# Kernel tuning notes

Measured on AMD Instinct MI355X. Metric: run time of the kernel, lower is better.

Reference implementation:

```python
import jax, jax.numpy as jnp
import numpy as np
import math

# dims matching init_kwargs
B, N, CS, CZ = 1, 512, 384, 128
H, C, PQ, PV = 8, 128, 8, 8
INF, EPS = 1e5, 1e-8

# ---- quaternion / motor helpers (PGA motor encoded as [qw,qx,qy,qz,tx,ty,tz,0]) ----

def quat_conj(q):
    return q * jnp.array([1.0, -1.0, -1.0, -1.0], q.dtype)

def quat_mul(a, b):
    aw, ax, ay, az = jnp.split(a, 4, -1)
    bw, bx, by, bz = jnp.split(b, 4, -1)
    return jnp.concatenate([
        aw*bw - ax*bx - ay*by - az*bz,
        aw*bx + ax*bw + ay*bz - az*by,
        aw*by - ax*bz + ay*bw + az*bx,
        aw*bz + ax*by - ay*bx + az*bw], -1)

def quat_rotate(q, v):
    qv = q[..., 1:]
    uv = jnp.cross(qv, v)
    uuv = jnp.cross(qv, uv)
    return v + 2.0 * (q[..., :1] * uv + uuv)

def point_trafo(p, q, t):
    # p [...,K,3]; rigid transform by frame motor, homogeneous 4-vector out
    pp = quat_rotate(q, p) + t
    return jnp.concatenate([pp, jnp.ones_like(pp[..., :1])], -1)

def mv_transform(mv, q, t):
    # versor sandwich on a 16-dim multivector: three rotatable 3-vector blocks,
    # the point block (7:10, weight at 10) also translates; slots 0 and 10:16 invariant
    s0 = mv[..., 0:1]
    v1 = quat_rotate(q, mv[..., 1:4])
    v2 = quat_rotate(q, mv[..., 4:7])
    w = mv[..., 10:11]
    p = quat_rotate(q, mv[..., 7:10]) + w * t
    return jnp.concatenate([s0, v1, v2, p, mv[..., 10:16]], -1)

def mv_transform_inv(mv, q, t):
    qc = quat_conj(q)
    s0 = mv[..., 0:1]
    v1 = quat_rotate(qc, mv[..., 1:4])
    v2 = quat_rotate(qc, mv[..., 4:7])
    w = mv[..., 10:11]
    p = quat_rotate(qc, mv[..., 7:10] - w * t)
    return jnp.concatenate([s0, v1, v2, p, mv[..., 10:16]], -1)


def _forward(s, g, z, T, mask, W_q, b_q, W_kv, b_kv, W_qp, b_qp, W_kp, b_kp,
             W_vg, b_vg, W_mg, W_b, b_b, W_dz, b_dz, head_weights,
             softmax_weights, W_out, b_out, W_geo):
    T8 = T[..., :8]                                      # extract_motor
    qn = T8[..., :4]
    qn = qn / jnp.sqrt(jnp.sum(qn**2, -1, keepdims=True) + EPS)
    tr = T8[..., 4:7]

    q = (s @ W_q + b_q).reshape(B, N, H, C)
    kv = (s @ W_kv + b_kv).reshape(B, N, H, 2 * C)
    k, v = kv[..., :C], kv[..., C:]

    def make_pts(W, bb):
        # split into 3 chunks + stack(dim=-1) == reshape(...,3,HP).swapaxes
        p = (s @ W + bb).reshape(B, N, 3, H * PQ).swapaxes(-1, -2)  # [B,N,HP,3]
        p4 = point_trafo(p, qn[:, :, None, :], tr[:, :, None, :])
        return p4.reshape(B, N, H, PQ, 4)

    q_pts = make_pts(W_qp, b_qp)
    k_pts = make_pts(W_kp, b_kp)

    v_g = (s @ W_vg + b_vg).reshape(B, N, PV, 16)
    v_g = jnp.einsum('oi,bnic->bnoc', W_mg,
                     jnp.concatenate([v_g, g], -2)).reshape(B, N, H, PV, 16)

    bias = jnp.einsum('bijz,zh->bhij', z, W_b) + b_b[None, :, None, None]
    a = jnp.einsum('bihc,bjhc->bhij', q, k) * math.sqrt(1.0 / (3 * C))
    a = a + math.sqrt(1.0 / 3.0) * bias

    disp = q_pts[:, :, None, :, :, :3] - k_pts[:, None, :, :, :, :3]  # [B,N,N,H,P,3]
    pt = jnp.sum(disp**2, -1)                                         # [B,N,N,H,P]
    hw = jax.nn.softplus(head_weights) * math.sqrt(1.0 / (3 * (PQ * 9.0 / 2)))
    pt = -0.5 * jnp.sum(pt * hw[None, None, None, :, None], -1)       # [B,N,N,H]

    sq_mask = INF * (mask[:, :, None] * mask[:, None, :] - 1.0)
    a = a + pt.transpose(0, 3, 1, 2) + sq_mask[:, None]
    a = jax.nn.softmax(softmax_weights[None, :, None, None] * a, axis=-1)

    o = jnp.einsum('bhij,bjhc->bihc', a, v)                           # [B,N,H,C]

    qb, tb = qn[:, :, None, None, :], tr[:, :, None, None, :]
    vg_glob = mv_transform(v_g, qb, tb)
    o_g = jnp.einsum('bhij,bjhpc->bihpc', a, vg_glob)
    o_g = mv_transform_inv(o_g, qb, tb)                               # [B,N,H,PV,16]
    n1 = jnp.sqrt(jnp.sum(o_g[..., :10]**2, -1) + EPS)
    n2 = jnp.sqrt(jnp.sum(o_g[..., 10:]**2, -1) + EPS)
    o_g_norm = jnp.stack([n1, n2], -1)                                # [B,N,H,PV,2]

    # local relative frame features (8 per head)
    q_rel = quat_mul(quat_conj(qn)[:, :, None, :], qn[:, None, :, :])
    t_rel = quat_rotate(quat_conj(qn)[:, :, None, :], tr[:, None, :, :] - tr[:, :, None, :])
    rel = jnp.concatenate([q_rel, t_rel, jnp.zeros_like(t_rel[..., :1])], -1)  # [B,N,N,8]
    o_rel = jnp.einsum('bhij,bijc->bihc', a, rel)

    o_pair = jnp.einsum('bhij,bijc->bihc', a, z @ W_dz + b_dz)        # [B,N,H,CZ//4]

    feats = jnp.concatenate([o_pair, o, o_rel,
                             o_g.reshape(B, N, H, PV * 16),
                             o_g_norm.reshape(B, N, H, PV * 2)], -1).reshape(B, N, -1)
    s_out = feats @ W_out + b_out                                     # [B,N,CS]
    g_out = jnp.einsum('oi,bnic->bnoc', W_geo, o_g.reshape(B, N, H * PV, 16))
    return s_out, g_out


def setup_inputs() -> dict:
    key = jax.random.key(0)
    ks = jax.random.split(key, 32)
    def rn(i, shape, sc=1.0):
        return sc * jax.random.normal(ks[i], shape, jnp.float32)
    s = rn(0, (B, N, CS))
    g = rn(1, (B, N, PV, 16))
    z = rn(2, (B, N, N, CZ))
    Traw = rn(3, (B, N, 16))
    qn = Traw[..., :4]
    qn = qn / jnp.sqrt(jnp.sum(qn**2, -1, keepdims=True) + 1e-8)
    T = Traw.at[..., :4].set(qn).at[..., 4:7].multiply(3.0).at[..., 7:].set(0.0)
    mask = jnp.ones((B, N), jnp.float32)
    w = 0.02
    CAT = H * (CZ // 4 + C + 8 + PV * 18)   # 2496
    return dict(
        s=s, g=g, z=z, T=T, mask=mask,
        W_q=rn(4, (CS, H * C), w), b_q=jnp.zeros((H * C,), jnp.float32),
        W_kv=rn(5, (CS, 2 * H * C), w), b_kv=jnp.zeros((2 * H * C,), jnp.float32),
        W_qp=rn(6, (CS, H * PQ * 3), w), b_qp=jnp.zeros((H * PQ * 3,), jnp.float32),
        W_kp=rn(7, (CS, H * PQ * 3), w), b_kp=jnp.zeros((H * PQ * 3,), jnp.float32),
        W_vg=rn(8, (CS, PV * 16), w), b_vg=jnp.zeros((PV * 16,), jnp.float32),
        W_mg=rn(9, (H * PV, 2 * PV), 0.1),
        W_b=rn(10, (CZ, H), w), b_b=jnp.zeros((H,), jnp.float32),
        W_dz=rn(11, (CZ, CZ // 4), w), b_dz=jnp.zeros((CZ // 4,), jnp.float32),
        head_weights=-2.0 + 0.3 * rn(12, (H,)),
        softmax_weights=jnp.ones((H,), jnp.float32) + 0.1 * rn(13, (H,)),
        W_out=rn(14, (CAT, CS), w), b_out=jnp.zeros((CS,), jnp.float32),
        W_geo=rn(15, (PV, H * PV), 0.1))


def reference(s, g, z, T, mask, W_q, b_q, W_kv, b_kv, W_qp, b_qp, W_kp, b_kp,
              W_vg, b_vg, W_mg, W_b, b_b, W_dz, b_dz, head_weights,
              softmax_weights, W_out, b_out, W_geo):
    return _forward(s, g, z, T, mask, W_q, b_q, W_kv, b_kv, W_qp, b_qp, W_kp,
                    b_kp, W_vg, b_vg, W_mg, W_b, b_b, W_dz, b_dz, head_weights,
                    softmax_weights, W_out, b_out, W_geo)
```

## Files before the change

### kernel.cpp

```cpp
#include <hip/hip_runtime.h>
#include <math.h>

#define NN 512
#define CSD 384
#define CZD 128
#define HD 8
#define CD 128
#define EPSV 1e-8f
#define INFV 100000.0f

#define OFF_QN    ((size_t)0)
#define OFF_TR    ((size_t)2048)
#define OFF_ROWT  ((size_t)4096)
#define OFF_COLT  ((size_t)8192)
#define OFF_SB    ((size_t)12288)
#define OFF_QBUF  ((size_t)45056)
#define OFF_KV    ((size_t)569344)
#define OFF_QPR   ((size_t)1617920)
#define OFF_KPR   ((size_t)1716224)
#define OFF_VGR   ((size_t)1814528)
#define OFF_ZB    ((size_t)1880064)
#define OFF_A     ((size_t)3977216)
#define OFF_AMH   ((size_t)6074368)
#define OFF_AML   ((size_t)7122944)
#define OFF_UH    ((size_t)8171520)
#define OFF_UL    ((size_t)8499200)
#define OFF_VH    ((size_t)8826880)
#define OFF_VL    ((size_t)9154560)
#define OFF_VPH   ((size_t)9482240)
#define OFF_VPL   ((size_t)10006528)
#define OFF_OB0   ((size_t)10530816)
#define OFF_OB1   ((size_t)11055104)
#define OFF_OG0   ((size_t)11579392)
#define OFF_OG1   ((size_t)12103680)
#define OFF_FH    ((size_t)12627968)
#define OFF_FL    ((size_t)13266944)
#define OFF_PS    ((size_t)13905920)
#define OFF_SH    ((size_t)15085568)
#define OFF_SL    ((size_t)15183872)
#define OFF_WTH   ((size_t)15282176)
#define OFF_WTL   ((size_t)15970304)
#define OFF_WOH   ((size_t)16658432)
#define OFF_WOL   ((size_t)17137664)

typedef __attribute__((ext_vector_type(4))) float f32x4;
typedef __attribute__((ext_vector_type(8))) short bf16x8;
typedef __attribute__((ext_vector_type(4))) short s16x4;
typedef unsigned short u16;

__device__ __forceinline__ void qrot(const float q[4], const float* v, float* out) {
    float qw = q[0], qx = q[1], qy = q[2], qz = q[3];
    float ux = qy*v[2] - qz*v[1];
    float uy = qz*v[0] - qx*v[2];
    float uz = qx*v[1] - qy*v[0];
    float uux = qy*uz - qz*uy;
    float uuy = qz*ux - qx*uz;
    float uuz = qx*uy - qy*ux;
    out[0] = v[0] + 2.0f*(qw*ux + uux);
    out[1] = v[1] + 2.0f*(qw*uy + uuy);
    out[2] = v[2] + 2.0f*(qw*uz + uuz);
}

__device__ __forceinline__ void cvt2(float x, u16& h, u16& lo) {
    unsigned u = __float_as_uint(x);
    unsigned r = (u + 0x7FFFu + ((u >> 16) & 1u)) >> 16;
    h = (u16)r;
    float hf = __uint_as_float(r << 16);
    float lf = x - hf;
    unsigned u2 = __float_as_uint(lf);
    unsigned r2 = (u2 + 0x7FFFu + ((u2 >> 16) & 1u)) >> 16;
    lo = (u16)r2;
}
__device__ __forceinline__ float bf2f(u16 h) { return __uint_as_float((unsigned)h << 16); }

#define MFMA3(acc, avh, avl, bvh, bvl) \
    acc = __builtin_amdgcn_mfma_f32_16x16x32_bf16(avh, bvh, acc, 0, 0, 0); \
    acc = __builtin_amdgcn_mfma_f32_16x16x32_bf16(avh, bvl, acc, 0, 0, 0); \
    acc = __builtin_amdgcn_mfma_f32_16x16x32_bf16(avl, bvh, acc, 0, 0, 0);


__global__ __launch_bounds__(256) void k_split(
    const float* __restrict__ s, const float* __restrict__ W_q, const float* __restrict__ W_kv,
    const float* __restrict__ W_qp, const float* __restrict__ W_kp, const float* __restrict__ W_vg,
    const float* __restrict__ W_out,
    u16* __restrict__ sh_, u16* __restrict__ sl_,
    u16* __restrict__ WTh, u16* __restrict__ WTl,
    u16* __restrict__ WOh, u16* __restrict__ WOl)
{
    __shared__ float tile[64*68];
    int task = blockIdx.z, bx = blockIdx.x, by = blockIdx.y, t = threadIdx.x;
    if (task == 0) {
        if (by >= 6) return;
        const float* W; int ldn, sn0;
        if (bx < 16)      { W = W_q;  ldn = 1024; sn0 = bx*64; }
        else if (bx < 48) { W = W_kv; ldn = 2048; sn0 = (bx-16)*64; }
        else if (bx < 51) { W = W_qp; ldn = 192;  sn0 = (bx-48)*64; }
        else if (bx < 54) { W = W_kp; ldn = 192;  sn0 = (bx-51)*64; }
        else              { W = W_vg; ldn = 128;  sn0 = (bx-54)*64; }
        int k0 = by*64;
        #pragma unroll
        for (int lp = 0; lp < 4; lp++) {
            int kk = (t>>4) + lp*16, nn = (t&15)*4;
            float4 v = *(const float4*)(W + (size_t)(k0+kk)*ldn + sn0 + nn);
            tile[kk*68+nn]=v.x; tile[kk*68+nn+1]=v.y; tile[kk*68+nn+2]=v.z; tile[kk*68+nn+3]=v.w;
        }
        __syncthreads();
        #pragma unroll
        for (int lp = 0; lp < 4; lp++) {
            int nn = (t>>4) + lp*16, kk4 = (t&15)*4;
            s16x4 vh, vl;
            #pragma unroll
            for (int e = 0; e < 4; e++) {
                u16 h, lo; cvt2(tile[(kk4+e)*68 + nn], h, lo);
                vh[e] = (short)h; vl[e] = (short)lo;
            }
            size_t o = (size_t)(bx*64 + nn)*384 + k0 + kk4;
            *(s16x4*)(WTh + o) = vh;
            *(s16x4*)(WTl + o) = vl;
        }
    } else if (task == 1) {
        if (bx >= 6 || by >= 39) return;
        int n0 = bx*64, k0 = by*64;
        #pragma unroll
        for (int lp = 0; lp < 4; lp++) {
            int kk = (t>>4) + lp*16, nn = (t&15)*4;
            float4 v = *(const float4*)(W_out + (size_t)(k0+kk)*384 + n0 + nn);
            tile[kk*68+nn]=v.x; tile[kk*68+nn+1]=v.y; tile[kk*68+nn+2]=v.z; tile[kk*68+nn+3]=v.w;
        }
        __syncthreads();
        #pragma unroll
        for (int lp = 0; lp < 4; lp++) {
            int nn = (t>>4) + lp*16, kk4 = (t&15)*4;
            s16x4 vh, vl;
            #pragma unroll
            for (int e = 0; e < 4; e++) {
                u16 h, lo; cvt2(tile[(kk4+e)*68 + nn], h, lo);
                vh[e] = (short)h; vl[e] = (short)lo;
            }
            size_t o = (size_t)(n0 + nn)*2496 + k0 + kk4;
            *(s16x4*)(WOh + o) = vh;
            *(s16x4*)(WOl + o) = vl;
        }
    } else {
        if (bx >= 8 || by >= 6) return;
        int m0 = bx*64, k0 = by*64;
        #pragma unroll
        for (int lp = 0; lp < 4; lp++) {
            int row = (t>>4) + lp*16, c4 = (t&15)*4;
            float4 v = *(const float4*)(s + (size_t)(m0+row)*384 + k0 + c4);
            s16x4 vh, vl;
            u16 h, lo;
            cvt2(v.x,h,lo); vh[0]=(short)h; vl[0]=(short)lo;
            cvt2(v.y,h,lo); vh[1]=(short)h; vl[1]=(short)lo;
            cvt2(v.z,h,lo); vh[2]=(short)h; vl[2]=(short)lo;
            cvt2(v.w,h,lo); vh[3]=(short)h; vl[3]=(short)lo;
            size_t o = (size_t)(m0+row)*384 + k0 + c4;
            *(s16x4*)(sh_ + o) = vh;
            *(s16x4*)(sl_ + o) = vl;
        }
    }
}

__global__ __launch_bounds__(256) void k_proj_all(
    const u16* __restrict__ sh_, const u16* __restrict__ sl_,
    const u16* __restrict__ WTh, const u16* __restrict__ WTl,
    const float* __restrict__ b_q,  float* __restrict__ qbuf,
    const float* __restrict__ b_kv, float* __restrict__ kvb,
    const float* __restrict__ b_qp, float* __restrict__ qpr,
    const float* __restrict__ b_kp, float* __restrict__ kpr,
    const float* __restrict__ b_vg, float* __restrict__ vgr)
{
    int ny = blockIdx.y;
    const float* bias; float* C; int N, n0, base;
    if (ny < 16)      { bias=b_q;  C=qbuf; N=1024; n0=ny*64;      base=0; }
    else if (ny < 48) { bias=b_kv; C=kvb;  N=2048; n0=(ny-16)*64; base=1024; }
    else if (ny < 51) { bias=b_qp; C=qpr;  N=192;  n0=(ny-48)*64; base=3072; }
    else if (ny < 54) { bias=b_kp; C=kpr;  N=192;  n0=(ny-51)*64; base=3264; }
    else              { bias=b_vg; C=vgr;  N=128;  n0=(ny-54)*64; base=3456; }
    int m0 = blockIdx.x*64;
    int t = threadIdx.x, w = t>>6, l = t&63, g = l>>4, li = l&15;
    const u16* Ah = sh_ + (size_t)(m0 + w*16 + li)*384 + g*8;
    const u16* Al = sl_ + (size_t)(m0 + w*16 + li)*384 + g*8;
    const u16* Bh0 = WTh + (size_t)(base + n0 + li)*384 + g*8;
    const u16* Bl0 = WTl + (size_t)(base + n0 + li)*384 + g*8;
    f32x4 acc[4] = {};
    for (int ks = 0; ks < 12; ks++) {
        bf16x8 avh = *(const bf16x8*)(Ah + ks*32);
        bf16x8 avl = *(const bf16x8*)(Al + ks*32);
        #pragma unroll
        for (int c = 0; c < 4; c++) {
            bf16x8 bvh = *(const bf16x8*)(Bh0 + (size_t)c*16*384 + ks*32);
            bf16x8 bvl = *(const bf16x8*)(Bl0 + (size_t)c*16*384 + ks*32);
            MFMA3(acc[c], avh, avl, bvh, bvl);
        }
    }
    #pragma unroll
    for (int c = 0; c < 4; c++) {
        int col = n0 + c*16 + li;
        float bb = bias[col];
        #pragma unroll
        for (int r = 0; r < 4; r++) {
            int row = m0 + w*16 + g*4 + r;
            C[(size_t)row*N + col] = acc[c][r] + bb;
        }
    }
}

__global__ __launch_bounds__(256) void k_geo(
    const float* __restrict__ T,
    const float* __restrict__ qpr, const float* __restrict__ kpr,
    const float* __restrict__ vgr, const float* __restrict__ g,
    const float* __restrict__ W_mg,
    const float* __restrict__ qbuf, const float* __restrict__ kvb,
    const float* __restrict__ hwraw, const float* __restrict__ b_b,
    float* __restrict__ qn, float* __restrict__ tr,
    u16* __restrict__ Uh, u16* __restrict__ Ul,
    u16* __restrict__ Vh, u16* __restrict__ Vl,
    float* __restrict__ rowt, float* __restrict__ colt,
    u16* __restrict__ Vph, u16* __restrict__ Vpl)
{
    __shared__ float s_q[4];
    __shared__ float s_t[3];
    __shared__ float s_qpts[192], s_kpts[192];
    __shared__ float s_Qsq[8], s_Ksq[8];
    int n = blockIdx.x, t = threadIdx.x;
    if (t == 0) {
        float q0=T[n*16+0], q1=T[n*16+1], q2=T[n*16+2], q3=T[n*16+3];
        float inv = 1.0f/sqrtf(q0*q0+q1*q1+q2*q2+q3*q3 + EPSV);
        float a0=q0*inv, a1=q1*inv, a2=q2*inv, a3=q3*inv;
        s_q[0]=a0; s_q[1]=a1; s_q[2]=a2; s_q[3]=a3;
        float u0=T[n*16+4], u1=T[n*16+5], u2=T[n*16+6];
        s_t[0]=u0; s_t[1]=u1; s_t[2]=u2;
        qn[n*4+0]=a0; qn[n*4+1]=a1; qn[n*4+2]=a2; qn[n*4+3]=a3;
        tr[n*3+0]=u0; tr[n*3+1]=u1; tr[n*3+2]=u2;
    }
    __syncthreads();
    float q[4]={s_q[0],s_q[1],s_q[2],s_q[3]};
    float t0=s_t[0], t1=s_t[1], t2=s_t[2];
    if (t < 128) {
        int m = t & 63;
        const float* raw = (t < 64) ? qpr : kpr;
        float p[3] = {raw[n*192 + m], raw[n*192 + 64 + m], raw[n*192 + 128 + m]};
        float r[3]; qrot(q,p,r);
        r[0]+=t0; r[1]+=t1; r[2]+=t2;
        float* dp = (t<64) ? s_qpts : s_kpts;
        dp[m*3+0]=r[0]; dp[m*3+1]=r[1]; dp[m*3+2]=r[2];
        float ss = r[0]*r[0]+r[1]*r[1]+r[2]*r[2];
        ss += __shfl_down(ss,4,8);
        ss += __shfl_down(ss,2,8);
        ss += __shfl_down(ss,1,8);
        if ((m&7)==0) ((t<64)?s_Qsq:s_Ksq)[m>>3] = ss;
    } else if (t < 192) {
        int o = t - 128;
        float in[16];
        #pragma unroll
        for (int c=0;c<16;c++){
            float acc=0.0f;
            #pragma unroll
            for (int i=0;i<8;i++)  acc += W_mg[o*16+i]*vgr[n*128+i*16+c];
            #pragma unroll
            for (int i=8;i<16;i++) acc += W_mg[o*16+i]*g[n*128+(i-8)*16+c];
            in[c]=acc;
        }
        float out[16];
        out[0]=in[0];
        qrot(q,in+1,out+1);
        qrot(q,in+4,out+4);
        float w=in[10];
        qrot(q,in+7,out+7);
        out[7]+=w*t0; out[8]+=w*t1; out[9]+=w*t2;
        #pragma unroll
        for (int c=10;c<16;c++) out[c]=in[c];
        int h=o>>3, pp=o&7;
        size_t vb = ((size_t)(h*512+n))*256 + 128 + pp*16;
        #pragma unroll
        for (int c=0;c<16;c++) {
            u16 hh, ll; cvt2(out[c], hh, ll);
            Vph[vb+c]=hh; Vpl[vb+c]=ll;
        }
    }
    #pragma unroll
    for (int l=0;l<4;l++){
        int f = t + l*256; int h = f>>7, c = f&127;
        u16 hh, ll; cvt2(kvb[(size_t)n*2048 + h*256 + 128 + c], hh, ll);
        Vph[((size_t)(h*512+n))*256 + c] = hh;
        Vpl[((size_t)(h*512+n))*256 + c] = ll;
    }
    __syncthreads();
    #pragma unroll
    for (int h = 0; h < 8; h++) {
        float hwv = log1pf(expf(hwraw[h])) * 0.09622504486493763f;
        if (t < 160) {
            float u, v;
            if (t < 128) {
                u = 0.05103103630798287f * qbuf[(size_t)n*1024 + h*128 + t];
                v = kvb[(size_t)n*2048 + h*256 + t];
            } else if (t < 152) {
                int d = t - 128;
                u = hwv * s_qpts[h*24 + d];
                v = s_kpts[h*24 + d];
            } else { u = 0.0f; v = 0.0f; }
            size_t o = ((size_t)h*512 + n)*160 + t;
            u16 hh, ll;
            cvt2(u, hh, ll); Uh[o]=hh; Ul[o]=ll;
            cvt2(v, hh, ll); Vh[o]=hh; Vl[o]=ll;
        }
        if (t == 160) rowt[h*512+n] = -0.5f*hwv*s_Qsq[h] + 0.5773502691896258f*b_b[h] - INFV;
        if (t == 161) colt[h*512+n] = -0.5f*hwv*s_Ksq[h];
    }
}

__global__ __launch_bounds__(128) void k_zb(const float* __restrict__ z,
        const float* __restrict__ W_b, float* __restrict__ zb) {
    __shared__ float zt[64*132];
    __shared__ float part[8*64];
    int i = blockIdx.x, j0 = blockIdx.y*64;
    int t = threadIdx.x;
    #pragma unroll
    for (int l = 0; l < 16; l++) {
        int f = t + l*128;
        int row = f >> 5, c4 = (f & 31) << 2;
        float4 v = *(const float4*)(z + ((size_t)(i*NN) + j0 + row)*CZD + c4);
        *(float4*)(zt + row*132 + c4) = v;
    }
    __syncthreads();
    int w = t >> 6, j = t & 63;
    int cbase = w*64;
    float acc[8] = {};
    #pragma unroll
    for (int c16 = 0; c16 < 16; c16++) {
        float4 v = *(const float4*)(zt + j*132 + cbase + c16*4);
        int c = cbase + c16*4;
        #pragma unroll
        for (int h = 0; h < 8; h++)
            acc[h] += v.x*W_b[(c+0)*8+h] + v.y*W_b[(c+1)*8+h]
                    + v.z*W_b[(c+2)*8+h] + v.w*W_b[(c+3)*8+h];
    }
    if (w == 1) {
        #pragma unroll
        for (int h = 0; h < 8; h++) part[h*64 + j] = acc[h];
    }
    __syncthreads();
    if (w == 0) {
        #pragma unroll
        for (int h = 0; h < 8; h++)
            zb[((size_t)h*512 + i)*512 + j0 + j] = acc[h] + part[h*64 + j];
    }
}

__global__ __launch_bounds__(256) void k_scorefill(
        const u16* __restrict__ Uh, const u16* __restrict__ Ul,
        const u16* __restrict__ Vh, const u16* __restrict__ Vl,
        const float* __restrict__ rowt, const float* __restrict__ colt,
        const float* __restrict__ zb, const float* __restrict__ mask,
        const float* __restrict__ sw, float* __restrict__ Am) {
    int h = blockIdx.z;
    int m0 = blockIdx.x*64, n0 = blockIdx.y*64;
    int t = threadIdx.x, w = t>>6, l = t&63, g = l>>4, li = l&15;
    const u16* Ah = Uh + ((size_t)h*512 + m0 + w*16 + li)*160 + g*8;
    const u16* Al = Ul + ((size_t)h*512 + m0 + w*16 + li)*160 + g*8;
    const u16* Bh0 = Vh + ((size_t)h*512 + n0 + li)*160 + g*8;
    const u16* Bl0 = Vl + ((size_t)h*512 + n0 + li)*160 + g*8;
    f32x4 acc[4] = {};
    #pragma unroll
    for (int ks = 0; ks < 5; ks++) {
        bf16x8 avh = *(const bf16x8*)(Ah + ks*32);
        bf16x8 avl = *(const bf16x8*)(Al + ks*32);
        #pragma unroll
        for (int c = 0; c < 4; c++) {
            bf16x8 bvh = *(const bf16x8*)(Bh0 + (size_t)c*16*160 + ks*32);
            bf16x8 bvl = *(const bf16x8*)(Bl0 + (size_t)c*16*160 + ks*32);
            MFMA3(acc[c], avh, avl, bvh, bvl);
        }
    }
    float swh = sw[h];
    #pragma unroll
    for (int c = 0; c < 4; c++) {
        int j = n0 + c*16 + li;
        float ct = colt[h*512 + j];
        float mj = mask[j];
        #pragma unroll
        for (int r = 0; r < 4; r++) {
            int i = m0 + w*16 + g*4 + r;
            float rt = rowt[h*512 + i];
            float mi = mask[i]*INFV;
            float zv = zb[((size_t)h*512 + i)*512 + j];
            Am[((size_t)h*512 + i)*512 + j] =
                (acc[c][r] + rt + ct + 0.5773502691896258f*zv + mi*mj)*swh;
        }
    }
}

__global__ __launch_bounds__(256) void k_softmax(const float* __restrict__ Am,
        u16* __restrict__ Amh, u16* __restrict__ Aml,
        const float* __restrict__ qn, const float* __restrict__ tr, float* __restrict__ S) {
    __shared__ float red[8];
    __shared__ float sred[4][8];
    int row = blockIdx.x;
    const float* p = Am + (size_t)row*512;
    int t = threadIdx.x;
    float x0 = p[t], x1 = p[t+256];
    float m = fmaxf(x0, x1);
    #pragma unroll
    for (int o = 32; o > 0; o >>= 1) m = fmaxf(m, __shfl_xor(m, o));
    int wv = t >> 6, ln = t & 63;
    if (ln == 0) red[wv] = m;
    __syncthreads();
    m = fmaxf(fmaxf(red[0], red[1]), fmaxf(red[2], red[3]));
    float e0 = expf(x0 - m), e1 = expf(x1 - m);
    float sm = e0 + e1;
    #pragma unroll
    for (int o = 32; o > 0; o >>= 1) sm += __shfl_xor(sm, o);
    __syncthreads();
    if (ln == 0) red[4 + wv] = sm;
    __syncthreads();
    float inv = 1.0f / (red[4]+red[5]+red[6]+red[7]);
    float a0 = e0*inv, a1 = e1*inv;
    u16 hh, ll;
    cvt2(a0, hh, ll); Amh[(size_t)row*512 + t] = hh;     Aml[(size_t)row*512 + t] = ll;
    cvt2(a1, hh, ll); Amh[(size_t)row*512 + t+256] = hh; Aml[(size_t)row*512 + t+256] = ll;
    float4 q0 = *(const float4*)(qn + t*4);
    float4 q1 = *(const float4*)(qn + (t+256)*4);
    float acc[8];
    acc[0] = a0*q0.x + a1*q1.x;
    acc[1] = a0*q0.y + a1*q1.y;
    acc[2] = a0*q0.z + a1*q1.z;
    acc[3] = a0*q0.w + a1*q1.w;
    acc[4] = a0*tr[t*3+0] + a1*tr[(t+256)*3+0];
    acc[5] = a0*tr[t*3+1] + a1*tr[(t+256)*3+1];
    acc[6] = a0*tr[t*3+2] + a1*tr[(t+256)*3+2];
    acc[7] = a0 + a1;
    #pragma unroll
    for (int c = 0; c < 8; c++) {
        #pragma unroll
        for (int o = 32; o > 0; o >>= 1) acc[c] += __shfl_xor(acc[c], o);
    }
    if (ln == 0) {
        #pragma unroll
        for (int c = 0; c < 8; c++) sred[wv][c] = acc[c];
    }
    __syncthreads();
    if (t < 8) {
        int h = row >> 9, i = row & 511;
        S[i*64 + h*8 + t] = sred[0][t]+sred[1][t]+sred[2][t]+sred[3][t];
    }
}

__global__ __launch_bounds__(256) void k_apply(
        const u16* __restrict__ Amh, const u16* __restrict__ Aml,
        const u16* __restrict__ Vph, const u16* __restrict__ Vpl,
        float* __restrict__ ob0, float* __restrict__ ob1,
        float* __restrict__ og0, float* __restrict__ og1) {
    __shared__ u16 sBh[2][64*48];
    __shared__ u16 sBl[2][64*48];
    int m0 = blockIdx.x*64;
    int n0 = blockIdx.y*64;
    int h = blockIdx.z & 7, js = blockIdx.z >> 3;
    int t = threadIdx.x, w = t>>6, l = t&63, g = l>>4, li = l&15;
    int jl = t>>3, c8 = (t&7)*8;
    int jsw = jl ^ (((c8>>3)&3)<<3);
    const u16* Ah = Amh + ((size_t)h*512 + m0 + w*16 + li)*512 + js*256 + g*8;
    const u16* Al = Aml + ((size_t)h*512 + m0 + w*16 + li)*512 + js*256 + g*8;
    f32x4 acc[4] = {};
    {
        const u16* srcH = Vph + ((size_t)h*512 + js*256 + jl)*256 + n0 + c8;
        const u16* srcL = Vpl + ((size_t)h*512 + js*256 + jl)*256 + n0 + c8;
        bf16x8 vh = *(const bf16x8*)srcH;
        bf16x8 vl = *(const bf16x8*)srcL;
        #pragma unroll
        for (int e = 0; e < 8; e++) {
            sBh[0][(c8+e)*48 + jsw] = (u16)vh[e];
            sBl[0][(c8+e)*48 + jsw] = (u16)vl[e];
        }
    }
    __syncthreads();
    for (int kc = 0; kc < 8; kc++) {
        int cur = kc & 1;
        if (kc + 1 < 8) {
            int koff = js*256 + (kc+1)*32;
            const u16* srcH = Vph + ((size_t)h*512 + koff + jl)*256 + n0 + c8;
            const u16* srcL = Vpl + ((size_t)h*512 + koff + jl)*256 + n0 + c8;
            bf16x8 vh = *(const bf16x8*)srcH;
            bf16x8 vl = *(const bf16x8*)srcL;
            #pragma unroll
            for (int e = 0; e < 8; e++) {
                sBh[cur^1][(c8+e)*48 + jsw] = (u16)vh[e];
                sBl[cur^1][(c8+e)*48 + jsw] = (u16)vl[e];
            }
        }
        bf16x8 avh = *(const bf16x8*)(Ah + kc*32);
        bf16x8 avl = *(const bf16x8*)(Al + kc*32);
        #pragma unroll
        for (int c = 0; c < 4; c++) {
            int col = c*16 + li;
            int gp = g ^ ((col>>3)&3);
            bf16x8 bvh = *(const bf16x8*)(&sBh[cur][col*48 + gp*8]);
            bf16x8 bvl = *(const bf16x8*)(&sBl[cur][col*48 + gp*8]);
            MFMA3(acc[c], avh, avl, bvh, bvl);
        }
        __syncthreads();
    }
    float* obuf = js ? ob1 : ob0;
    float* og   = js ? og1 : og0;
    #pragma unroll
    for (int c = 0; c < 4; c++) {
        int col = n0 + c*16 + li;
        float* base = (col < 128) ? (obuf + h*128 + col) : (og + h*128 + col - 128);
        #pragma unroll
        for (int r = 0; r < 4; r++) {
            int i = m0 + w*16 + g*4 + r;
            base[(size_t)i*1024] = acc[c][r];
        }
    }
}

__global__ __launch_bounds__(256) void k_azfin(
    const u16* __restrict__ Amh, const u16* __restrict__ Aml, const float* __restrict__ z,
    const float* __restrict__ ob0, const float* __restrict__ ob1,
    const float* __restrict__ og0, const float* __restrict__ og1,
    const float* __restrict__ W_dz, const float* __restrict__ b_dz,
    const float* __restrict__ S, const float* __restrict__ qn, const float* __restrict__ tr,
    const float* __restrict__ W_geo,
    u16* __restrict__ fh, u16* __restrict__ fl, float* __restrict__ outg)
{
    __shared__ float aT[512*8];
    __shared__ float part[3*1024];
    __shared__ float s_az[1024];
    __shared__ float s_og[1024];
    int i = blockIdx.x, t = threadIdx.x;
    #pragma unroll
    for (int l = 0; l < 16; l++) {
        int f = t + l*256;
        int h = f >> 9, j = f & 511;
        size_t idx = ((size_t)h*512 + i)*512 + j;
        aT[j*8 + h] = bf2f(Amh[idx]) + bf2f(Aml[idx]);
    }
    __syncthreads();
    int c2 = t & 63, quarter = t >> 6;
    int jb = quarter*128;
    float acc[8][2] = {};
    for (int j = jb; j < jb+128; j++) {
        float2 zv = *(const float2*)(z + ((size_t)(i*NN) + j)*CZD + c2*2);
        float4 a0 = *(const float4*)(aT + j*8);
        float4 a1 = *(const float4*)(aT + j*8 + 4);
        acc[0][0] += a0.x*zv.x; acc[0][1] += a0.x*zv.y;
        acc[1][0] += a0.y*zv.x; acc[1][1] += a0.y*zv.y;
        acc[2][0] += a0.z*zv.x; acc[2][1] += a0.z*zv.y;
        acc[3][0] += a0.w*zv.x; acc[3][1] += a0.w*zv.y;
        acc[4][0] += a1.x*zv.x; acc[4][1] += a1.x*zv.y;
        acc[5][0] += a1.y*zv.x; acc[5][1] += a1.y*zv.y;
        acc[6][0] += a1.z*zv.x; acc[6][1] += a1.z*zv.y;
        acc[7][0] += a1.w*zv.x; acc[7][1] += a1.w*zv.y;
    }
    if (quarter > 0) {
        #pragma unroll
        for (int h = 0; h < 8; h++) {
            part[(quarter-1)*1024 + h*128 + c2*2 + 0] = acc[h][0];
            part[(quarter-1)*1024 + h*128 + c2*2 + 1] = acc[h][1];
        }
    }
    __syncthreads();
    if (quarter == 0) {
        #pragma unroll
        for (int h = 0; h < 8; h++) {
            #pragma unroll
            for (int d = 0; d < 2; d++) {
                s_az[h*128 + c2*2 + d] = acc[h][d] + part[h*128 + c2*2 + d]
                          + part[1024 + h*128 + c2*2 + d] + part[2048 + h*128 + c2*2 + d];
            }
        }
    }
    __syncthreads();
    size_t fb = (size_t)i*2496;
    u16 hh, ll;
    #pragma unroll
    for (int l = 0; l < 4; l++) {
        int ff = t + l*256; int h = ff>>7, c = ff&127;
        float v = ob0[(size_t)i*1024 + h*128 + c] + ob1[(size_t)i*1024 + h*128 + c];
        cvt2(v, hh, ll); fh[fb + h*312 + 32 + c] = hh; fl[fb + h*312 + 32 + c] = ll;
    }
    {
        int h = t >> 5, cdz = t & 31;
        float a2 = b_dz[cdz];
        #pragma unroll 4
        for (int zc = 0; zc < 128; zc++) a2 += s_az[h*128 + zc]*W_dz[zc*32 + cdz];
        cvt2(a2, hh, ll); fh[fb + h*312 + cdz] = hh; fl[fb + h*312 + cdz] = ll;
    }
    float qc0=qn[i*4], qc1=-qn[i*4+1], qc2=-qn[i*4+2], qc3=-qn[i*4+3];
    float t0=tr[i*3], t1=tr[i*3+1], t2=tr[i*3+2];
    if (t < 64) {
        int h = t >> 3, p = t & 7;
        const float* a0 = og0 + (size_t)i*1024 + h*128 + p*16;
        const float* a1 = og1 + (size_t)i*1024 + h*128 + p*16;
        float in[16];
        #pragma unroll
        for (int c=0;c<16;c++) in[c]=a0[c]+a1[c];
        float qc[4]={qc0,qc1,qc2,qc3};
        float out[16];
        out[0]=in[0];
        qrot(qc,in+1,out+1);
        qrot(qc,in+4,out+4);
        float w=in[10];
        float tmp[3]={in[7]-w*t0, in[8]-w*t1, in[9]-w*t2};
        qrot(qc,tmp,out+7);
        #pragma unroll
        for (int c2x=10;c2x<16;c2x++) out[c2x]=in[c2x];
        float n1=EPSV, n2=EPSV;
        #pragma unroll
        for (int c2x=0;c2x<10;c2x++) n1 += out[c2x]*out[c2x];
        #pragma unroll
        for (int c2x=10;c2x<16;c2x++) n2 += out[c2x]*out[c2x];
        n1=sqrtf(n1); n2=sqrtf(n2);
        #pragma unroll
        for (int c2x=0;c2x<16;c2x++){
            cvt2(out[c2x], hh, ll);
            fh[fb + h*312+168+p*16+c2x] = hh; fl[fb + h*312+168+p*16+c2x] = ll;
            s_og[t*16+c2x]=out[c2x];
        }
        cvt2(n1, hh, ll); fh[fb + h*312+296+p*2]   = hh; fl[fb + h*312+296+p*2]   = ll;
        cvt2(n2, hh, ll); fh[fb + h*312+296+p*2+1] = hh; fl[fb + h*312+296+p*2+1] = ll;
    } else if (t < 72) {
        int h = t - 64;
        const float* Sr = S + i*64 + h*8;
        float b0=Sr[0], b1=Sr[1], b2=Sr[2], b3=Sr[3];
        float o0 = qc0*b0 - qc1*b1 - qc2*b2 - qc3*b3;
        float o1 = qc0*b1 + qc1*b0 + qc2*b3 - qc3*b2;
        float o2 = qc0*b2 - qc1*b3 + qc2*b0 + qc3*b1;
        float o3 = qc0*b3 + qc1*b2 - qc2*b1 + qc3*b0;
        float A = Sr[7];
        float v[3]={Sr[4]-A*t0, Sr[5]-A*t1, Sr[6]-A*t2};
        float qc[4]={qc0,qc1,qc2,qc3};
        float r[3]; qrot(qc,v,r);
        cvt2(o0,hh,ll);  fh[fb+h*312+160]=hh; fl[fb+h*312+160]=ll;
        cvt2(o1,hh,ll);  fh[fb+h*312+161]=hh; fl[fb+h*312+161]=ll;
        cvt2(o2,hh,ll);  fh[fb+h*312+162]=hh; fl[fb+h*312+162]=ll;
        cvt2(o3,hh,ll);  fh[fb+h*312+163]=hh; fl[fb+h*312+163]=ll;
        cvt2(r[0],hh,ll);fh[fb+h*312+164]=hh; fl[fb+h*312+164]=ll;
        cvt2(r[1],hh,ll);fh[fb+h*312+165]=hh; fl[fb+h*312+165]=ll;
        cvt2(r[2],hh,ll);fh[fb+h*312+166]=hh; fl[fb+h*312+166]=ll;
        fh[fb+h*312+167]=0; fl[fb+h*312+167]=0;
    }
    __syncthreads();
    if (t < 128) {
        int o = (t>>4) & 7, c = t & 15;
        float a3 = 0.0f;
        #pragma unroll 4
        for (int i2=0;i2<64;i2++) a3 += W_geo[o*64+i2]*s_og[i2*16+c];
        outg[(size_t)i*128 + o*16 + c] = a3;
    }
}

__global__ __launch_bounds__(256) void k_sout(
        const u16* __restrict__ fh, const u16* __restrict__ fl,
        const u16* __restrict__ WOh, const u16* __restrict__ WOl,
        float* __restrict__ Ps) {
    int m0 = blockIdx.x*64, n0 = blockIdx.y*64, kz = blockIdx.z;
    int t = threadIdx.x, w = t>>6, l = t&63, g = l>>4, li = l&15;
    const u16* Ah = fh + (size_t)(m0 + w*16 + li)*2496 + kz*416 + g*8;
    const u16* Al = fl + (size_t)(m0 + w*16 + li)*2496 + kz*416 + g*8;
    const u16* Bh0 = WOh + (size_t)(n0 + li)*2496 + kz*416 + g*8;
    const u16* Bl0 = WOl + (size_t)(n0 + li)*2496 + kz*416 + g*8;
    f32x4 acc[4] = {};
    for (int ks = 0; ks < 13; ks++) {
        bf16x8 avh = *(const bf16x8*)(Ah + ks*32);
        bf16x8 avl = *(const bf16x8*)(Al + ks*32);
        #pragma unroll
        for (int c = 0; c < 4; c++) {
            bf16x8 bvh = *(const bf16x8*)(Bh0 + (size_t)c*16*2496 + ks*32);
            bf16x8 bvl = *(const bf16x8*)(Bl0 + (size_t)c*16*2496 + ks*32);
            MFMA3(acc[c], avh, avl, bvh, bvl);
        }
    }
    float* slab = Ps + (size_t)kz*512*384;
    #pragma unroll
    for (int c = 0; c < 4; c++) {
        int col = n0 + c*16 + li;
        #pragma unroll
        for (int r = 0; r < 4; r++) {
            int row = m0 + w*16 + g*4 + r;
            slab[(size_t)row*CSD + col] = acc[c][r];
        }
    }
}

__global__ __launch_bounds__(256) void k_sout_red(const float* __restrict__ Ps,
        const float* __restrict__ b_out, float* __restrict__ out) {
    int idx = (blockIdx.x*256 + threadIdx.x)*4;
    float4 s = *(const float4*)(b_out + (idx % 384));
    #pragma unroll
    for (int kz = 0; kz < 6; kz++) {
        float4 p = *(const float4*)(Ps + (size_t)kz*196608 + idx);
        s.x += p.x; s.y += p.y; s.z += p.z; s.w += p.w;
    }
    *(float4*)(out + idx) = s;
}


extern "C" void kernel_launch(void* const* d_in, const int* in_sizes, int n_in,
                              void* d_out, int out_size, void* d_ws, size_t ws_size,
                              hipStream_t stream) {
    const float* s     = (const float*)d_in[0];
    const float* g     = (const float*)d_in[1];
    const float* z     = (const float*)d_in[2];
    const float* T     = (const float*)d_in[3];
    const float* mask  = (const float*)d_in[4];
    const float* W_q   = (const float*)d_in[5];
    const float* b_q   = (const float*)d_in[6];
    const float* W_kv  = (const float*)d_in[7];
    const float* b_kv  = (const float*)d_in[8];
    const float* W_qp  = (const float*)d_in[9];
    const float* b_qp  = (const float*)d_in[10];
    const float* W_kp  = (const float*)d_in[11];
    const float* b_kp  = (const float*)d_in[12];
    const float* W_vg  = (const float*)d_in[13];
    const float* b_vg  = (const float*)d_in[14];
    const float* W_mg  = (const float*)d_in[15];
    const float* W_b   = (const float*)d_in[16];
    const float* b_b   = (const float*)d_in[17];
    const float* W_dz  = (const float*)d_in[18];
    const float* b_dz  = (const float*)d_in[19];
    const float* hw    = (const float*)d_in[20];
    const float* sw    = (const float*)d_in[21];
    const float* W_out = (const float*)d_in[22];
    const float* b_out = (const float*)d_in[23];
    const float* W_geo = (const float*)d_in[24];

    float* ws   = (float*)d_ws;
    float* out  = (float*)d_out;

    float* qn   = ws + OFF_QN;
    float* tr   = ws + OFF_TR;
    float* rowt = ws + OFF_ROWT;
    float* colt = ws + OFF_COLT;
    float* Sbuf = ws + OFF_SB;
    float* qbuf = ws + OFF_QBUF;
    float* kvb  = ws + OFF_KV;
    float* qpr  = ws + OFF_QPR;
    float* kpr  = ws + OFF_KPR;
    float* vgr  = ws + OFF_VGR;
    float* zb   = ws + OFF_ZB;
    float* Am   = ws + OFF_A;
    u16* Amh    = (u16*)(ws + OFF_AMH);
    u16* Aml    = (u16*)(ws + OFF_AML);
    u16* Uh     = (u16*)(ws + OFF_UH);
    u16* Ul     = (u16*)(ws + OFF_UL);
    u16* Vh     = (u16*)(ws + OFF_VH);
    u16* Vl     = (u16*)(ws + OFF_VL);
    u16* Vph    = (u16*)(ws + OFF_VPH);
    u16* Vpl    = (u16*)(ws + OFF_VPL);
    float* ob0  = ws + OFF_OB0;
    float* ob1  = ws + OFF_OB1;
    float* og0  = ws + OFF_OG0;
    float* og1  = ws + OFF_OG1;
    u16* fh     = (u16*)(ws + OFF_FH);
    u16* fl     = (u16*)(ws + OFF_FL);
    float* Ps   = ws + OFF_PS;
    u16* sh_    = (u16*)(ws + OFF_SH);
    u16* sl_    = (u16*)(ws + OFF_SL);
    u16* WTh    = (u16*)(ws + OFF_WTH);
    u16* WTl    = (u16*)(ws + OFF_WTL);
    u16* WOh    = (u16*)(ws + OFF_WOH);
    u16* WOl    = (u16*)(ws + OFF_WOL);

    k_split<<<dim3(56,39,3),256,0,stream>>>(s,W_q,W_kv,W_qp,W_kp,W_vg,W_out,
                                            sh_,sl_,WTh,WTl,WOh,WOl);
    k_proj_all<<<dim3(8,56),256,0,stream>>>(sh_,sl_,WTh,WTl,
                                            b_q,qbuf, b_kv,kvb, b_qp,qpr, b_kp,kpr, b_vg,vgr);
    k_geo<<<NN,256,0,stream>>>(T,qpr,kpr,vgr,g,W_mg,qbuf,kvb,hw,b_b,
                               qn,tr,Uh,Ul,Vh,Vl,rowt,colt,Vph,Vpl);
    k_zb<<<dim3(NN,8),128,0,stream>>>(z,W_b,zb);
    k_scorefill<<<dim3(8,8,8),256,0,stream>>>(Uh,Ul,Vh,Vl,rowt,colt,zb,mask,sw,Am);
    k_softmax<<<4096,256,0,stream>>>(Am,Amh,Aml,qn,tr,Sbuf);
    k_apply<<<dim3(8,4,16),256,0,stream>>>(Amh,Aml,Vph,Vpl,ob0,ob1,og0,og1);
    k_azfin<<<NN,256,0,stream>>>(Amh,Aml,z,ob0,ob1,og0,og1,W_dz,b_dz,Sbuf,qn,tr,W_geo,
                                 fh,fl, out + (size_t)NN*CSD);
    k_sout<<<dim3(8,6,6),256,0,stream>>>(fh,fl,WOh,WOl,Ps);
    k_sout_red<<<192,256,0,stream>>>(Ps,b_out,out);
}
```

Measured before the change: 409.6 us.

## Split attention-weighted z reduction into parallel kernel and rework k_zb with register weights

The A·z reduction that k_azfin did in one block per row is moved into a new k_az kernel. It splits the j dimension into four chunks across a 512x4 grid and writes partial sums to a workspace buffer, which k_azfin then adds up. This raises parallelism on the largest z read, at the cost of an extra launch and a partial-sum round trip through memory. Separately, k_zb drops the shared-memory staging and keeps the W_b slice in registers, reducing with wavefront shuffles over 256-thread blocks.

```diff
diff --git a/kernel.cpp b/kernel.cpp
--- a/kernel.cpp
+++ b/kernel.cpp
@@ -42,6 +42,7 @@
 #define OFF_WTL   ((size_t)15970304)
 #define OFF_WOH   ((size_t)16658432)
 #define OFF_WOL   ((size_t)17137664)
+#define OFF_AZP   ((size_t)17616896)
 
 typedef __attribute__((ext_vector_type(4))) float f32x4;
 typedef __attribute__((ext_vector_type(8))) short bf16x8;
@@ -310,41 +311,33 @@
     }
 }
 
-__global__ __launch_bounds__(128) void k_zb(const float* __restrict__ z,
+__global__ __launch_bounds__(256) void k_zb(const float* __restrict__ z,
         const float* __restrict__ W_b, float* __restrict__ zb) {
-    __shared__ float zt[64*132];
-    __shared__ float part[8*64];
-    int i = blockIdx.x, j0 = blockIdx.y*64;
-    int t = threadIdx.x;
-    #pragma unroll
-    for (int l = 0; l < 16; l++) {
-        int f = t + l*128;
-        int row = f >> 5, c4 = (f & 31) << 2;
-        float4 v = *(const float4*)(z + ((size_t)(i*NN) + j0 + row)*CZD + c4);
-        *(float4*)(zt + row*132 + c4) = v;
-    }
-    __syncthreads();
-    int w = t >> 6, j = t & 63;
-    int cbase = w*64;
-    float acc[8] = {};
-    #pragma unroll
-    for (int c16 = 0; c16 < 16; c16++) {
-        float4 v = *(const float4*)(zt + j*132 + cbase + c16*4);
-        int c = cbase + c16*4;
-        #pragma unroll
-        for (int h = 0; h < 8; h++)
-            acc[h] += v.x*W_b[(c+0)*8+h] + v.y*W_b[(c+1)*8+h]
-                    + v.z*W_b[(c+2)*8+h] + v.w*W_b[(c+3)*8+h];
-    }
-    if (w == 1) {
-        #pragma unroll
-        for (int h = 0; h < 8; h++) part[h*64 + j] = acc[h];
-    }
-    __syncthreads();
-    if (w == 0) {
-        #pragma unroll
-        for (int h = 0; h < 8; h++)
-            zb[((size_t)h*512 + i)*512 + j0 + j] = acc[h] + part[h*64 + j];
+    int i = blockIdx.x, j0 = blockIdx.y*128;
+    int t = threadIdx.x, w = t>>6, l = t&63;
+    int jj = l>>5, c4 = (l&31)<<2;
+    float wb[4][8];
+    #pragma unroll
+    for (int e=0;e<4;e++)
+        #pragma unroll
+        for (int h=0;h<8;h++) wb[e][h] = W_b[(c4+e)*8 + h];
+    int jbase = j0 + w*32 + jj;
+    const float* zp = z + ((size_t)i*512 + jbase)*128 + c4;
+    for (int k = 0; k < 16; k++) {
+        float4 v = *(const float4*)(zp + (size_t)k*256);
+        float acc[8];
+        #pragma unroll
+        for (int h=0;h<8;h++)
+            acc[h] = v.x*wb[0][h] + v.y*wb[1][h] + v.z*wb[2][h] + v.w*wb[3][h];
+        #pragma unroll
+        for (int h=0;h<8;h++) {
+            #pragma unroll
+            for (int m=16;m>0;m>>=1) acc[h] += __shfl_xor(acc[h], m);
+        }
+        if ((l&31) < 8) {
+            int h = l&31;
+            zb[((size_t)h*512 + i)*512 + jbase + k*2] = acc[h];
+        }
     }
 }
 
@@ -443,6 +436,59 @@
     if (t < 8) {
         int h = row >> 9, i = row & 511;
         S[i*64 + h*8 + t] = sred[0][t]+sred[1][t]+sred[2][t]+sred[3][t];
+    }
+}
+
+__global__ __launch_bounds__(256) void k_az(
+        const u16* __restrict__ Amh, const u16* __restrict__ Aml,
+        const float* __restrict__ z, float* __restrict__ azp) {
+    __shared__ float aT[128*12];
+    __shared__ float part[3*1024];
+    int i = blockIdx.x, jq = blockIdx.y, j0 = jq*128;
+    int t = threadIdx.x;
+    #pragma unroll
+    for (int l2 = 0; l2 < 4; l2++) {
+        int f = t + l2*256;
+        int h = f >> 7, jl = f & 127;
+        size_t idx = ((size_t)h*512 + i)*512 + j0 + jl;
+        aT[jl*12 + h] = bf2f(Amh[idx]) + bf2f(Aml[idx]);
+    }
+    __syncthreads();
+    int c2 = t & 63, sub = t >> 6;
+    int jb = sub*32;
+    float acc[8][2] = {};
+    for (int jo = 0; jo < 32; jo++) {
+        int j = jb + jo;
+        float2 zv = *(const float2*)(z + ((size_t)i*512 + j0 + j)*128 + c2*2);
+        float4 a0 = *(const float4*)(aT + j*12);
+        float4 a1 = *(const float4*)(aT + j*12 + 4);
+        acc[0][0] += a0.x*zv.x; acc[0][1] += a0.x*zv.y;
+        acc[1][0] += a0.y*zv.x; acc[1][1] += a0.y*zv.y;
+        acc[2][0] += a0.z*zv.x; acc[2][1] += a0.z*zv.y;
+        acc[3][0] += a0.w*zv.x; acc[3][1] += a0.w*zv.y;
+        acc[4][0] += a1.x*zv.x; acc[4][1] += a1.x*zv.y;
+        acc[5][0] += a1.y*zv.x; acc[5][1] += a1.y*zv.y;
+        acc[6][0] += a1.z*zv.x; acc[6][1] += a1.z*zv.y;
+        acc[7][0] += a1.w*zv.x; acc[7][1] += a1.w*zv.y;
+    }
+    if (sub > 0) {
+        #pragma unroll
+        for (int h = 0; h < 8; h++) {
+            part[(sub-1)*1024 + h*128 + c2*2 + 0] = acc[h][0];
+            part[(sub-1)*1024 + h*128 + c2*2 + 1] = acc[h][1];
+        }
+    }
+    __syncthreads();
+    if (sub == 0) {
+        float* dst = azp + ((size_t)jq*512 + i)*1024;
+        #pragma unroll
+        for (int h = 0; h < 8; h++) {
+            #pragma unroll
+            for (int d = 0; d < 2; d++) {
+                dst[h*128 + c2*2 + d] = acc[h][d] + part[h*128 + c2*2 + d]
+                          + part[1024 + h*128 + c2*2 + d] + part[2048 + h*128 + c2*2 + d];
+            }
+        }
     }
 }
 
@@ -515,7 +561,7 @@
 }
 
 __global__ __launch_bounds__(256) void k_azfin(
-    const u16* __restrict__ Amh, const u16* __restrict__ Aml, const float* __restrict__ z,
+    const float* __restrict__ azp,
     const float* __restrict__ ob0, const float* __restrict__ ob1,
     const float* __restrict__ og0, const float* __restrict__ og1,
     const float* __restrict__ W_dz, const float* __restrict__ b_dz,
@@ -523,52 +569,14 @@
     const float* __restrict__ W_geo,
     u16* __restrict__ fh, u16* __restrict__ fl, float* __restrict__ outg)
 {
-    __shared__ float aT[512*8];
-    __shared__ float part[3*1024];
     __shared__ float s_az[1024];
     __shared__ float s_og[1024];
     int i = blockIdx.x, t = threadIdx.x;
     #pragma unroll
-    for (int l = 0; l < 16; l++) {
-        int f = t + l*256;
-        int h = f >> 9, j = f & 511;
-        size_t idx = ((size_t)h*512 + i)*512 + j;
-        aT[j*8 + h] = bf2f(Amh[idx]) + bf2f(Aml[idx]);
-    }
-    __syncthreads();
-    int c2 = t & 63, quarter = t >> 6;
-    int jb = quarter*128;
-    float acc[8][2] = {};
-    for (int j = jb; j < jb+128; j++) {
-        float2 zv = *(const float2*)(z + ((size_t)(i*NN) + j)*CZD + c2*2);
-        float4 a0 = *(const float4*)(aT + j*8);
-        float4 a1 = *(const float4*)(aT + j*8 + 4);
-        acc[0][0] += a0.x*zv.x; acc[0][1] += a0.x*zv.y;
-        acc[1][0] += a0.y*zv.x; acc[1][1] += a0.y*zv.y;
-        acc[2][0] += a0.z*zv.x; acc[2][1] += a0.z*zv.y;
-        acc[3][0] += a0.w*zv.x; acc[3][1] += a0.w*zv.y;
-        acc[4][0] += a1.x*zv.x; acc[4][1] += a1.x*zv.y;
-        acc[5][0] += a1.y*zv.x; acc[5][1] += a1.y*zv.y;
-        acc[6][0] += a1.z*zv.x; acc[6][1] += a1.z*zv.y;
-        acc[7][0] += a1.w*zv.x; acc[7][1] += a1.w*zv.y;
-    }
-    if (quarter > 0) {
-        #pragma unroll
-        for (int h = 0; h < 8; h++) {
-            part[(quarter-1)*1024 + h*128 + c2*2 + 0] = acc[h][0];
-            part[(quarter-1)*1024 + h*128 + c2*2 + 1] = acc[h][1];
-        }
-    }
-    __syncthreads();
-    if (quarter == 0) {
-        #pragma unroll
-        for (int h = 0; h < 8; h++) {
-            #pragma unroll
-            for (int d = 0; d < 2; d++) {
-                s_az[h*128 + c2*2 + d] = acc[h][d] + part[h*128 + c2*2 + d]
-                          + part[1024 + h*128 + c2*2 + d] + part[2048 + h*128 + c2*2 + d];
-            }
-        }
+    for (int l2 = 0; l2 < 4; l2++) {
+        int c = t + l2*256;
+        s_az[c] = azp[((size_t)0*512 + i)*1024 + c] + azp[((size_t)1*512 + i)*1024 + c]
+                + azp[((size_t)2*512 + i)*1024 + c] + azp[((size_t)3*512 + i)*1024 + c];
     }
     __syncthreads();
     size_t fb = (size_t)i*2496;
@@ -761,6 +769,7 @@
     u16* WTl    = (u16*)(ws + OFF_WTL);
     u16* WOh    = (u16*)(ws + OFF_WOH);
     u16* WOl    = (u16*)(ws + OFF_WOL);
+    float* azp  = ws + OFF_AZP;
 
     k_split<<<dim3(56,39,3),256,0,stream>>>(s,W_q,W_kv,W_qp,W_kp,W_vg,W_out,
                                             sh_,sl_,WTh,WTl,WOh,WOl);
@@ -768,11 +777,12 @@
                                             b_q,qbuf, b_kv,kvb, b_qp,qpr, b_kp,kpr, b_vg,vgr);
     k_geo<<<NN,256,0,stream>>>(T,qpr,kpr,vgr,g,W_mg,qbuf,kvb,hw,b_b,
                                qn,tr,Uh,Ul,Vh,Vl,rowt,colt,Vph,Vpl);
-    k_zb<<<dim3(NN,8),128,0,stream>>>(z,W_b,zb);
+    k_zb<<<dim3(512,4),256,0,stream>>>(z,W_b,zb);
     k_scorefill<<<dim3(8,8,8),256,0,stream>>>(Uh,Ul,Vh,Vl,rowt,colt,zb,mask,sw,Am);
     k_softmax<<<4096,256,0,stream>>>(Am,Amh,Aml,qn,tr,Sbuf);
+    k_az<<<dim3(512,4),256,0,stream>>>(Amh,Aml,z,azp);
     k_apply<<<dim3(8,4,16),256,0,stream>>>(Amh,Aml,Vph,Vpl,ob0,ob1,og0,og1);
-    k_azfin<<<NN,256,0,stream>>>(Amh,Aml,z,ob0,ob1,og0,og1,W_dz,b_dz,Sbuf,qn,tr,W_geo,
+    k_azfin<<<NN,256,0,stream>>>(azp,ob0,ob1,og0,og1,W_dz,b_dz,Sbuf,qn,tr,W_geo,
                                  fh,fl, out + (size_t)NN*CSD);
     k_sout<<<dim3(8,6,6),256,0,stream>>>(fh,fl,WOh,WOl,Ps);
     k_sout_red<<<192,256,0,stream>>>(Ps,b_out,out);
```

Measured after the change: 415.5 us. Within noise of the previous version (+1.4%).
